# Performance work log

Measured on AMD Instinct MI355X. Metric: run time of the kernel, lower is better.

Reference implementation:

```python
import jax, jax.numpy as jnp
import numpy as np

N_PRIMES = 50
BATCH = 4096
DIM = 8192
GOLDEN_RATIO = (1.0 + np.sqrt(5.0)) / 2.0


def _generate_primes(n):
    primes = []
    num = 2
    while len(primes) < n:
        if all(num % p != 0 for p in primes):
            primes.append(num)
        num += 1
    return np.array(primes, dtype=np.int32)


def setup_inputs() -> dict:
    key = jax.random.key(0)
    k1, k2, k3 = jax.random.split(key, 3)
    return {
        "token_hash": jax.random.randint(k3, (BATCH,), 0, 1000000000, dtype=jnp.int32),
        "primes": jnp.asarray(_generate_primes(N_PRIMES)),  # [50] int32, constant
        "resonance_scales": jax.random.normal(k1, (N_PRIMES,), dtype=jnp.float32),
        "phase_shifts": jax.random.normal(k2, (N_PRIMES,), dtype=jnp.float32),
        "energy_preservation": jnp.asarray(1.0, dtype=jnp.float32),
        "dimension": DIM,
    }


def reference(token_hash, primes, resonance_scales, phase_shifts, energy_preservation, dimension):
    n_primes = primes.shape[0]
    idx = jnp.arange(dimension) % n_primes                      # [D] prime index per spectrum slot
    p = primes[idx].astype(jnp.float32)                         # [D]
    base_freq = p * (GOLDEN_RATIO * np.pi / dimension)          # [D]
    scale = jax.nn.sigmoid(resonance_scales[idx])               # [D]
    freq = base_freq * scale * energy_preservation              # [D]
    # token modulation: (token_hash % 1000) / 1000
    tm = (token_hash % 1000).astype(jnp.float32) / 1000.0       # [B]
    angle = phase_shifts[idx][None, :] + tm[:, None] * (2.0 * np.pi)  # [B, D]
    spectrum = freq[None, :] * (1.0 + 0.1 * jnp.sin(angle))     # [B, D]
    norm = jnp.linalg.norm(spectrum, axis=-1, keepdims=True)    # [B, 1]
    spectrum = jnp.where(norm > 0, spectrum * energy_preservation / norm, spectrum)
    return spectrum
```

## Files before the change

### kernel.cpp

```cpp
#include <hip/hip_runtime.h>
#include <math.h>


#define PHI_PI 5.083203692315259f

__global__ __launch_bounds__(256) void phrs_kernel(
    const int*   __restrict__ token_hash,
    const int*   __restrict__ primes,
    const float* __restrict__ rscales,
    const float* __restrict__ pshifts,
    const float* __restrict__ energy,
    float*       __restrict__ out,
    int B, int D, int NP)
{
    __shared__ float  s_sn[64];
    __shared__ float4 s_pat[64];
    __shared__ float  s_inv;

    const int b   = blockIdx.x;
    const int tid = threadIdx.x;
    const float E = energy[0];

    if (tid < NP) {
        const float tm    = (float)(token_hash[b] % 1000) * 1e-3f;
        const float p     = (float)primes[tid];
        const float sig   = 1.0f / (1.0f + __expf(-rscales[tid]) * 0.0f + expf(-rscales[tid]) * 1.0f);
        const float freq  = p * (PHI_PI / (float)D) * sig * E;
        const float angle = pshifts[tid] + tm * 6.2831853071795864769f;
        s_sn[tid] = freq * (1.0f + 0.1f * sinf(angle));
    }
    __syncthreads();

    if (tid == 0) {
        const int q = D / NP, r = D % NP;
        float acc = 0.0f;
        for (int j = 0; j < NP; ++j) {
            float v = s_sn[j];
            float cnt = (float)(q + (j < r ? 1 : 0));
            acc += cnt * v * v;
        }
        float norm = sqrtf(acc);
        s_inv = (norm > 0.0f) ? (E / norm) : 1.0f;
    }
    __syncthreads();

    const float inv = s_inv;

    if ((D & 3) == 0) {
        int g = ((NP & 3) == 0) ? 4 : (((NP & 1) == 0) ? 2 : 1);
        const int PL = NP / g;
        for (int m = tid; m < PL; m += 256) {
            int e = 4 * m;
            float4 v;
            v.x = s_sn[(e    ) % NP] * inv;
            v.y = s_sn[(e + 1) % NP] * inv;
            v.z = s_sn[(e + 2) % NP] * inv;
            v.w = s_sn[(e + 3) % NP] * inv;
            s_pat[m] = v;
        }
        __syncthreads();

        float4* __restrict__ out4 = reinterpret_cast<float4*>(out);
        const int nv = D >> 2;
        const size_t rowbase = (size_t)b * (size_t)nv;
        int rmod = tid % PL;
        const int step = 256 % PL;
        for (int k = tid; k < nv; k += 256) {
            out4[rowbase + k] = s_pat[rmod];
            rmod += step;
            if (rmod >= PL) rmod -= PL;
        }
    } else {
        const size_t rowbase = (size_t)b * (size_t)D;
        for (int i = tid; i < D; i += 256) {
            out[rowbase + i] = s_sn[i % NP] * inv;
        }
    }
}

extern "C" void kernel_launch(void* const* d_in, const int* in_sizes, int n_in,
                              void* d_out, int out_size, void* d_ws, size_t ws_size,
                              hipStream_t stream) {
    const int*   token_hash = (const int*)  d_in[0];
    const int*   primes     = (const int*)  d_in[1];
    const float* rscales    = (const float*)d_in[2];
    const float* pshifts    = (const float*)d_in[3];
    const float* energy     = (const float*)d_in[4];
    float*       out        = (float*)      d_out;

    const int B  = in_sizes[0];
    const int NP = in_sizes[1];
    const int D  = out_size / B;

    phrs_kernel<<<dim3(B), dim3(256), 0, stream>>>(
        token_hash, primes, rscales, pshifts, energy, out, B, D, NP);
}
```

Measured before the change: 28.16 us.

## Map one wavefront per row with shuffle-based norm reduction

Each 256-thread block now handles four batch rows, one 64-lane wavefront per row, so the grid shrinks fourfold. The serial single-thread norm loop and its extra barrier are replaced by a wavefront xor-shuffle reduction. A specialised path for 50 primes with D divisible by 256 builds the float4 pattern and writes the row with an unrolled store loop. The aim is to cut per-block setup and synchronisation overhead in a store-bound kernel. The cost is that each wavefront now writes a whole row serially, and the fast path is hard-coded to the test's prime count.

```diff
diff --git a/kernel.cpp b/kernel.cpp
--- a/kernel.cpp
+++ b/kernel.cpp
@@ -2,7 +2,8 @@
 #include <math.h>
 
 
-#define PHI_PI 5.083203692315259f
+#define PHI_PI  5.083203692315259f
+#define TWO_PI  6.2831853071795864769f
 
 __global__ __launch_bounds__(256) void phrs_kernel(
     const int*   __restrict__ token_hash,
@@ -13,67 +14,70 @@
     float*       __restrict__ out,
     int B, int D, int NP)
 {
-    __shared__ float  s_sn[64];
-    __shared__ float4 s_pat[64];
-    __shared__ float  s_inv;
+    __shared__ float  s_raw[4][64];
+    __shared__ float4 s_pat[4][32];
 
-    const int b   = blockIdx.x;
-    const int tid = threadIdx.x;
-    const float E = energy[0];
+    const int w    = threadIdx.x >> 6;
+    const int lane = threadIdx.x & 63;
+    const int b    = blockIdx.x * 4 + w;
+    const float E  = energy[0];
 
-    if (tid < NP) {
+    float red = 0.0f;
+    if (b < B && lane < NP) {
         const float tm    = (float)(token_hash[b] % 1000) * 1e-3f;
-        const float p     = (float)primes[tid];
-        const float sig   = 1.0f / (1.0f + __expf(-rscales[tid]) * 0.0f + expf(-rscales[tid]) * 1.0f);
+        const float p     = (float)primes[lane];
+        const float sig   = 1.0f / (1.0f + expf(-rscales[lane]));
         const float freq  = p * (PHI_PI / (float)D) * sig * E;
-        const float angle = pshifts[tid] + tm * 6.2831853071795864769f;
-        s_sn[tid] = freq * (1.0f + 0.1f * sinf(angle));
+        const float angle = pshifts[lane] + tm * TWO_PI;
+        const float s     = freq * (1.0f + 0.1f * sinf(angle));
+        s_raw[w][lane] = s;
+        const int q = D / NP, r = D % NP;
+        red = (float)(q + (lane < r ? 1 : 0)) * s * s;
     }
+    #pragma unroll
+    for (int off = 32; off; off >>= 1)
+        red += __shfl_xor(red, off, 64);
+    const float inv = (red > 0.0f) ? (E / sqrtf(red)) : 1.0f;
+
     __syncthreads();
 
-    if (tid == 0) {
-        const int q = D / NP, r = D % NP;
-        float acc = 0.0f;
-        for (int j = 0; j < NP; ++j) {
-            float v = s_sn[j];
-            float cnt = (float)(q + (j < r ? 1 : 0));
-            acc += cnt * v * v;
-        }
-        float norm = sqrtf(acc);
-        s_inv = (norm > 0.0f) ? (E / norm) : 1.0f;
-    }
-    __syncthreads();
-
-    const float inv = s_inv;
-
-    if ((D & 3) == 0) {
-        int g = ((NP & 3) == 0) ? 4 : (((NP & 1) == 0) ? 2 : 1);
-        const int PL = NP / g;
-        for (int m = tid; m < PL; m += 256) {
-            int e = 4 * m;
+    if (NP == 50 && (D & 255) == 0) {
+        if (b < B && lane < 25) {
+            const int e = 4 * lane;
+            int i0 = e;     if (i0 >= 50) i0 -= 50;
+            int i1 = e + 1; if (i1 >= 50) i1 -= 50;
+            int i2 = e + 2; if (i2 >= 50) i2 -= 50;
+            int i3 = e + 3; if (i3 >= 50) i3 -= 50;
             float4 v;
-            v.x = s_sn[(e    ) % NP] * inv;
-            v.y = s_sn[(e + 1) % NP] * inv;
-            v.z = s_sn[(e + 2) % NP] * inv;
-            v.w = s_sn[(e + 3) % NP] * inv;
-            s_pat[m] = v;
+            v.x = s_raw[w][i0] * inv;
+            v.y = s_raw[w][i1] * inv;
+            v.z = s_raw[w][i2] * inv;
+            v.w = s_raw[w][i3] * inv;
+            s_pat[w][lane] = v;
         }
         __syncthreads();
 
-        float4* __restrict__ out4 = reinterpret_cast<float4*>(out);
-        const int nv = D >> 2;
-        const size_t rowbase = (size_t)b * (size_t)nv;
-        int rmod = tid % PL;
-        const int step = 256 % PL;
-        for (int k = tid; k < nv; k += 256) {
-            out4[rowbase + k] = s_pat[rmod];
-            rmod += step;
-            if (rmod >= PL) rmod -= PL;
+        if (b < B) {
+            float4* __restrict__ out4 = reinterpret_cast<float4*>(out);
+            const int nv = D >> 2;
+            const size_t base = (size_t)b * (size_t)nv;
+            int rmod = lane;
+            if (rmod >= 25) rmod -= 25;
+            if (rmod >= 25) rmod -= 25;
+            const int step = 64 % 25;
+            #pragma unroll 8
+            for (int k = lane; k < nv; k += 64) {
+                out4[base + k] = s_pat[w][rmod];
+                rmod += step;
+                if (rmod >= 25) rmod -= 25;
+            }
         }
     } else {
-        const size_t rowbase = (size_t)b * (size_t)D;
-        for (int i = tid; i < D; i += 256) {
-            out[rowbase + i] = s_sn[i % NP] * inv;
+        __syncthreads();
+        if (b < B) {
+            const size_t rowbase = (size_t)b * (size_t)D;
+            for (int i = lane; i < D; i += 64)
+                out[rowbase + i] = s_raw[w][i % NP] * inv;
         }
     }
 }
@@ -92,6 +96,7 @@
     const int NP = in_sizes[1];
     const int D  = out_size / B;
 
-    phrs_kernel<<<dim3(B), dim3(256), 0, stream>>>(
+    const int blocks = (B + 3) / 4;
+    phrs_kernel<<<dim3(blocks), dim3(256), 0, stream>>>(
         token_hash, primes, rscales, pshifts, energy, out, B, D, NP);
 }
```

New measurement: 26.92 us. 4.4% less time.
